# Kernel optimization log

Hardware: AMD Instinct MI355X
Metric: run time of the kernel (lower is better)

The kernel has to match this reference:

```python
import jax, jax.numpy as jnp
import numpy as np

K = 24            # kNN neighbors per DynamicEdgeConv (includes self, dist 0)
N_PER_GRAPH = 128 # uniform nodes per graph
N_GRAPHS = 128
N_IN = 16
HID = 128
N_OUT = 6


def _knn_idx(xg, k):
    # xg: [G, N, D] -> indices of k nearest neighbors per node, [G, N, k]
    sq = jnp.sum(xg * xg, axis=-1)                       # [G, N]
    d2 = sq[:, :, None] + sq[:, None, :] - 2.0 * jnp.einsum('gnd,gmd->gnm', xg, xg)
    _, idx = jax.lax.top_k(-d2, k)                       # smallest distances
    return idx


def _dynamic_edge_conv(xg, w, b, k=K):
    # DynamicEdgeConv: recompute kNN on current features, edge MLP on
    # [x_i, x_j - x_i], max-aggregate over neighbors.
    idx = _knn_idx(xg, k)                                # [G, N, k]
    x_j = jax.vmap(lambda v, i: v[i])(xg, idx)           # [G, N, k, D]
    x_i = xg[:, :, None, :]                              # [G, N, 1, D]
    e = jnp.concatenate([jnp.broadcast_to(x_i, x_j.shape), x_j - x_i], axis=-1)
    h = jax.nn.elu(jnp.einsum('gnkf,fh->gnkh', e, w) + b)
    return jnp.max(h, axis=2)                            # [G, N, H]


def _linear(x, w, b):
    return x @ w + b


def setup_inputs() -> dict:
    key = jax.random.key(0)
    ks = jax.random.split(key, 16)

    def W(k, fi, fo):
        return (jax.random.normal(k, (fi, fo), dtype=jnp.float32) / np.sqrt(fi)).astype(jnp.float32)

    inp = {
        'x_pf': jax.random.normal(ks[0], (N_GRAPHS * N_PER_GRAPH, N_IN), dtype=jnp.float32),
        'enc_w1': W(ks[1], N_IN, HID),  'enc_b1': jnp.zeros((HID,), jnp.float32),
        'enc_w2': W(ks[2], HID, HID),   'enc_b2': jnp.zeros((HID,), jnp.float32),
        'conv1_w': W(ks[3], 2 * HID, HID), 'conv1_b': jnp.zeros((HID,), jnp.float32),
        'conv2_w': W(ks[4], 2 * HID, HID), 'conv2_b': jnp.zeros((HID,), jnp.float32),
        'conv3_w': W(ks[5], 2 * HID, HID), 'conv3_b': jnp.zeros((HID,), jnp.float32),
        'out_w1': W(ks[6], HID, 64), 'out_b1': jnp.zeros((64,), jnp.float32),
        'out_w2': W(ks[7], 64, 32),  'out_b2': jnp.zeros((32,), jnp.float32),
        'out_w3': W(ks[8], 32, 32),  'out_b3': jnp.zeros((32,), jnp.float32),
        'out_w4': W(ks[9], 32, N_OUT), 'out_b4': jnp.zeros((N_OUT,), jnp.float32),
        'batch_pf': jnp.repeat(jnp.arange(N_GRAPHS, dtype=jnp.int64 if jax.config.jax_enable_x64 else jnp.int32), N_PER_GRAPH),
    }
    return inp


def reference(x_pf, enc_w1, enc_b1, enc_w2, enc_b2,
              conv1_w, conv1_b, conv2_w, conv2_b, conv3_w, conv3_b,
              out_w1, out_b1, out_w2, out_b2, out_w3, out_b3, out_w4, out_b4,
              batch_pf):
    G = x_pf.shape[0] // N_PER_GRAPH
    # pf_encode: Linear -> ELU -> Linear -> ELU
    h = jax.nn.elu(_linear(x_pf, enc_w1, enc_b1))
    h = jax.nn.elu(_linear(h, enc_w2, enc_b2))
    hg = h.reshape(G, N_PER_GRAPH, HID)  # uniform graphs; batch_pf = repeat(arange(G))
    hg = _dynamic_edge_conv(hg, conv1_w, conv1_b)
    hg = _dynamic_edge_conv(hg, conv2_w, conv2_b)
    hg = _dynamic_edge_conv(hg, conv3_w, conv3_b)
    # global_add_pool over nodes of each graph
    pooled = jnp.sum(hg, axis=1)                          # [G, HID]
    o = jax.nn.elu(_linear(pooled, out_w1, out_b1))
    o = jax.nn.elu(_linear(o, out_w2, out_b2))
    o = jax.nn.elu(_linear(o, out_w3, out_b3))
    o = _linear(o, out_w4, out_b4)
    return (o, batch_pf)
```

## Files before the change

### kernel.cpp

```cpp
#include <hip/hip_runtime.h>
#include <hip/hip_fp16.h>
#include <hip/hip_bf16.h>
#include <cmath>

#define G_NUM 128
#define NPTS  128
#define FDIM  128
#define KNNK  24
#define NTOT  (G_NUM*NPTS)

typedef short s8v __attribute__((ext_vector_type(8)));
typedef float f32x4 __attribute__((ext_vector_type(4)));

__device__ __forceinline__ float eluf(float x){ return x > 0.0f ? x : expm1f(x); }

__device__ __forceinline__ unsigned short f2bf(float f) {
    unsigned int u = __float_as_uint(f);
    unsigned int r = (u + 0x7fffu + ((u >> 16) & 1u)) >> 16;
    return (unsigned short)r;
}
__device__ __forceinline__ float bf2f(unsigned short b) {
    return __uint_as_float(((unsigned int)b) << 16);
}

__global__ void prep_kernel(const float* __restrict__ w1, const float* __restrict__ w2,
                            const float* __restrict__ w3, const float* __restrict__ ew2,
                            const float* __restrict__ b1, const float* __restrict__ b2,
                            const float* __restrict__ b3,
                            unsigned short* __restrict__ wcatT,
                            unsigned short* __restrict__ enc2T,
                            float* __restrict__ bias,
                            const int* __restrict__ bpf,
                            float* __restrict__ out)
{
    int e = blockIdx.x * 256 + threadIdx.x;
    if (e < 16384) out[768 + e] = (float)bpf[e];
    if (e < 98304) {
        int l = e >> 15;
        int r = e & 32767;
        int k = r >> 8;
        int n = r & 255;
        const float* w = (l == 0) ? w1 : ((l == 1) ? w2 : w3);
        float v = (n < 128) ? (w[k * 128 + n] - w[(128 + k) * 128 + n])
                            : w[(128 + k) * 128 + (n - 128)];
        wcatT[l * 32768 + n * 128 + k] = f2bf(v);
    } else if (e < 114688) {
        int i = e - 98304;
        int k = i >> 7, n = i & 127;
        enc2T[n * 128 + k] = f2bf(ew2[k * 128 + n]);
    } else if (e < 115456) {
        int j = e - 114688;
        int l = j >> 8, c = j & 255;
        const float* b = (l == 0) ? b1 : ((l == 1) ? b2 : b3);
        bias[l * 256 + c] = (c < 128) ? b[c] : 0.0f;
    }
}

#define E_XS  0
#define E_W1  4352
#define E_A   12544
__global__ __launch_bounds__(512) void enc_fused(const float* __restrict__ x_pf,
                                                 const float* __restrict__ w1,
                                                 const float* __restrict__ b1,
                                                 const unsigned short* __restrict__ e2T,
                                                 const float* __restrict__ b2,
                                                 float* __restrict__ hout)
{
    __shared__ char smc[28928];
    float* xs  = (float*)(smc + E_XS);
    float* ws1 = (float*)(smc + E_W1);
    const int tid = threadIdx.x;
    const int m0 = blockIdx.x * 64;

    for (int e = tid; e < 1024; e += 512) {
        int m = e >> 4, k = e & 15;
        xs[m * 17 + k] = x_pf[(size_t)(m0 + m) * 16 + k];
    }
    for (int e = tid; e < 2048; e += 512) ws1[e] = w1[e];
    __syncthreads();

    {
        const int h = tid & 127, mg = tid >> 7;
        float bb = b1[h];
        #pragma unroll
        for (int i = 0; i < 16; ++i) {
            int m = mg * 16 + i;
            float a = bb;
            #pragma unroll
            for (int k = 0; k < 16; ++k) a += xs[m * 17 + k] * ws1[k * 128 + h];
            a = eluf(a);
            int byte = (m * 256 + h * 2) ^ ((m & 15) << 4);
            *reinterpret_cast<unsigned short*>(smc + E_A + byte) = f2bf(a);
        }
    }
    __syncthreads();

    {
        const int l = tid & 63, w = tid >> 6;
        const int lr = l & 15, lg = l >> 4;
        const int mt = w >> 1, nh = w & 1;
        f32x4 acc[4] = {};
        #pragma unroll
        for (int ks = 0; ks < 4; ++ks) {
            int row = mt * 16 + lr;
            int abyte = (row * 256 + ks * 64 + lg * 16) ^ ((row & 15) << 4);
            s8v a_f = *reinterpret_cast<const s8v*>(smc + E_A + abyte);
            #pragma unroll
            for (int ni = 0; ni < 4; ++ni) {
                int n = nh * 64 + ni * 16 + lr;
                s8v b = *reinterpret_cast<const s8v*>(e2T + n * 128 + ks * 32 + lg * 8);
                acc[ni] = __builtin_amdgcn_mfma_f32_16x16x32_bf16(a_f, b, acc[ni], 0, 0, 0);
            }
        }
        #pragma unroll
        for (int ni = 0; ni < 4; ++ni) {
            int n = nh * 64 + ni * 16 + lr;
            float bl = b2[n];
            #pragma unroll
            for (int q = 0; q < 4; ++q)
                hout[(size_t)(m0 + mt * 16 + lg * 4 + q) * 128 + n] = eluf(acc[ni][q] + bl);
        }
    }
}

__global__ __launch_bounds__(256) void cgemm(const float* __restrict__ A,
                                             const unsigned short* __restrict__ Bt,
                                             const float* __restrict__ bias,
                                             float* __restrict__ a_out,
                                             unsigned int* __restrict__ c16)
{
    extern __shared__ char smc[];
    const int tid = threadIdx.x;
    const int m0 = blockIdx.x * 128;
    const unsigned short* Btg = Bt + (size_t)blockIdx.y * 16384;

    for (int e = tid; e < 4096; e += 256) {
        int m = e >> 5, q = e & 31;
        float4 v = *reinterpret_cast<const float4*>(&A[(size_t)(m0 + m) * 128 + 4 * q]);
        ushort4 p;
        p.x = f2bf(v.x); p.y = f2bf(v.y); p.z = f2bf(v.z); p.w = f2bf(v.w);
        int byte = (m * 256 + q * 8) ^ ((m & 15) << 4);
        *reinterpret_cast<ushort4*>(smc + byte) = p;
    }
    for (int e = tid; e < 2048; e += 256) {
        int n = e >> 4, q = e & 15;
        uint4 v = *reinterpret_cast<const uint4*>(Btg + n * 128 + q * 8);
        int byte = (n * 256 + q * 16) ^ ((n & 15) << 4);
        *reinterpret_cast<uint4*>(smc + 32768 + byte) = v;
    }
    __syncthreads();

    const int l = tid & 63, w = tid >> 6;
    const int wr = w >> 1, wc = w & 1;
    const int lr = l & 15, lg = l >> 4;

    f32x4 acc[4][4] = {};
    #pragma unroll
    for (int ks = 0; ks < 4; ++ks) {
        s8v a_f[4], b_f[4];
        #pragma unroll
        for (int mi = 0; mi < 4; ++mi) {
            int row = wr * 64 + mi * 16 + lr;
            int byte = (row * 256 + ks * 64 + lg * 16) ^ ((row & 15) << 4);
            a_f[mi] = *reinterpret_cast<const s8v*>(smc + byte);
        }
        #pragma unroll
        for (int ni = 0; ni < 4; ++ni) {
            int n = wc * 64 + ni * 16 + lr;
            int byte = (n * 256 + ks * 64 + lg * 16) ^ ((n & 15) << 4);
            b_f[ni] = *reinterpret_cast<const s8v*>(smc + 32768 + byte);
        }
        #pragma unroll
        for (int mi = 0; mi < 4; ++mi)
            #pragma unroll
            for (int ni = 0; ni < 4; ++ni)
                acc[mi][ni] = __builtin_amdgcn_mfma_f32_16x16x32_bf16(
                    a_f[mi], b_f[ni], acc[mi][ni], 0, 0, 0);
    }

    if (blockIdx.y == 0) {
        float bl[4];
        #pragma unroll
        for (int ni = 0; ni < 4; ++ni) bl[ni] = bias[wc * 64 + ni * 16 + lr];
        #pragma unroll
        for (int mi = 0; mi < 4; ++mi) {
            int rbase = m0 + wr * 64 + mi * 16 + lg * 4;
            #pragma unroll
            for (int ni = 0; ni < 4; ++ni) {
                int col = wc * 64 + ni * 16 + lr;
                #pragma unroll
                for (int q = 0; q < 4; ++q)
                    a_out[(size_t)(rbase + q) * 128 + col] = acc[mi][ni][q] + bl[ni];
            }
        }
    } else {
        #pragma unroll
        for (int mi = 0; mi < 4; ++mi) {
            int rbase = m0 + wr * 64 + mi * 16 + lg * 4;
            #pragma unroll
            for (int ni = 0; ni < 4; ++ni) {
                int col = wc * 64 + ni * 16 + lr;
                #pragma unroll
                for (int q = 0; q < 4; ++q) {
                    float v = acc[mi][ni][q];
                    float p = __shfl_xor(v, 1);
                    if (!(lr & 1)) {
                        unsigned int u =
                            ((unsigned int)__half_as_ushort(__float2half(p)) << 16)
                          |  (unsigned int)__half_as_ushort(__float2half(v));
                        c16[(size_t)(rbase + q) * 64 + (col >> 1)] = u;
                    }
                }
            }
        }
    }
}

#define CV_XHI 0
#define CV_XLO 32768
#define CV_D   32768
#define CV_PP  (32768 + 16384)
#define CV_IDX (32768 + 24576)
#define CV_SQ  65536
#define CONV_LDS 66048

template<int POOL>
__global__ __launch_bounds__(512, 4) void conv_fused(const float* __restrict__ hin,
                                                     const float* __restrict__ a_buf,
                                                     const unsigned int* __restrict__ c16,
                                                     float* __restrict__ hout,
                                                     float* __restrict__ ppool)
{
    extern __shared__ char smc[];
    float* Sq = (float*)(smc + CV_SQ);
    unsigned char* idxL = (unsigned char*)(smc + CV_IDX);
    float* pp = (float*)(smc + CV_PP);

    const int bid = blockIdx.x;
    const int g   = (bid & 7) * 16 + (bid >> 5);
    const int sub = (bid >> 3) & 3;
    const int r0  = sub * 32;
    const int tid = threadIdx.x;
    const float* hg = hin + (size_t)g * NPTS * FDIM;
    float* og = hout + (size_t)g * NPTS * FDIM;

    {
        const int m = tid >> 2;
        const int k0 = (tid & 3) * 32;
        float sq = 0.f;
        #pragma unroll
        for (int i = 0; i < 8; ++i) {
            float4 v = *reinterpret_cast<const float4*>(&hg[m * 128 + k0 + 4 * i]);
            ushort4 hi, lo;
            hi.x = f2bf(v.x); lo.x = f2bf(v.x - bf2f(hi.x));
            hi.y = f2bf(v.y); lo.y = f2bf(v.y - bf2f(hi.y));
            hi.z = f2bf(v.z); lo.z = f2bf(v.z - bf2f(hi.z));
            hi.w = f2bf(v.w); lo.w = f2bf(v.w - bf2f(hi.w));
            sq += v.x * v.x + v.y * v.y + v.z * v.z + v.w * v.w;
            int byte = (m * 256 + (k0 + 4 * i) * 2) ^ ((m & 15) << 4);
            *reinterpret_cast<ushort4*>(smc + CV_XHI + byte) = hi;
            *reinterpret_cast<ushort4*>(smc + CV_XLO + byte) = lo;
        }
        sq += __shfl_xor(sq, 1);
        sq += __shfl_xor(sq, 2);
        if ((tid & 3) == 0) Sq[m] = sq;
    }
    __syncthreads();

    const int l = tid & 63, w = tid >> 6;
    const int lr = l & 15, lg = l >> 4;

    f32x4 acc[2] = {};
    const int rt = w & 1, ct0 = w >> 1;
    const int arow = r0 + rt * 16 + lr;
    const int aswz = (arow & 15) << 4;
    #pragma unroll
    for (int ks = 0; ks < 4; ++ks) {
        int abyte = (arow * 256 + ks * 64 + lg * 16) ^ aswz;
        s8v ahi = *reinterpret_cast<const s8v*>(smc + CV_XHI + abyte);
        s8v alo = *reinterpret_cast<const s8v*>(smc + CV_XLO + abyte);
        #pragma unroll
        for (int t = 0; t < 2; ++t) {
            int brow = (ct0 + 4 * t) * 16 + lr;
            int bbyte = (brow * 256 + ks * 64 + lg * 16) ^ ((brow & 15) << 4);
            s8v bhi = *reinterpret_cast<const s8v*>(smc + CV_XHI + bbyte);
            s8v blo = *reinterpret_cast<const s8v*>(smc + CV_XLO + bbyte);
            acc[t] = __builtin_amdgcn_mfma_f32_16x16x32_bf16(alo, bhi, acc[t], 0, 0, 0);
            acc[t] = __builtin_amdgcn_mfma_f32_16x16x32_bf16(ahi, blo, acc[t], 0, 0, 0);
            acc[t] = __builtin_amdgcn_mfma_f32_16x16x32_bf16(ahi, bhi, acc[t], 0, 0, 0);
        }
    }
    float sqa[4], sqc[2];
    #pragma unroll
    for (int q = 0; q < 4; ++q) sqa[q] = Sq[r0 + rt * 16 + lg * 4 + q];
    #pragma unroll
    for (int t = 0; t < 2; ++t) sqc[t] = Sq[(ct0 + 4 * t) * 16 + lr];
    __syncthreads();

    #pragma unroll
    for (int t = 0; t < 2; ++t) {
        int col = (ct0 + 4 * t) * 16 + lr;
        #pragma unroll
        for (int q = 0; q < 4; ++q) {
            int row = rt * 16 + lg * 4 + q;
            *reinterpret_cast<float*>(smc + CV_D + ((row * 512 + col * 4) ^ ((row & 7) << 4)))
                = sqa[q] + sqc[t] - 2.f * acc[t][q];
        }
    }
    __syncthreads();

    for (int r = w * 4; r < w * 4 + 4; ++r) {
        float2 cur = *reinterpret_cast<const float2*>(
            smc + CV_D + ((r * 512 + 8 * l) ^ ((r & 7) << 4)));
        unsigned int ub0 = __float_as_uint(cur.x);
        unsigned int ub1 = __float_as_uint(cur.y);
        unsigned int u0 = (ub0 & 0x80000000u) ? ~ub0 : (ub0 | 0x80000000u);
        unsigned int u1 = (ub1 & 0x80000000u) ? ~ub1 : (ub1 | 0x80000000u);

        bool c0 = true, c1 = true, in0 = false, in1 = false;
        int need = KNNK;
        for (int b = 31; b >= 0; --b) {
            bool z0 = c0 && !((u0 >> b) & 1u);
            bool z1 = c1 && !((u1 >> b) & 1u);
            int cnt = __popcll(__ballot(z0)) + __popcll(__ballot(z1));
            if (cnt > need) { c0 = z0; c1 = z1; }
            else if (cnt == need) { in0 |= z0; in1 |= z1; need = 0; break; }
            else { in0 |= z0; in1 |= z1; need -= cnt;
                   c0 = c0 && !z0; c1 = c1 && !z1; }
        }
        if (need > 0) {
            unsigned long long m0 = __ballot(c0), m1 = __ballot(c1);
            unsigned long long below = (1ull << l) - 1ull;
            int rk0 = __popcll(m0 & below) + __popcll(m1 & below);
            int rk1 = rk0 + (int)((m0 >> l) & 1ull);
            in0 = in0 || (c0 && rk0 < need);
            in1 = in1 || (c1 && rk1 < need);
        }
        unsigned long long f0 = __ballot(in0), f1 = __ballot(in1);
        int cnt0 = __popcll(f0);
        unsigned long long below = (1ull << l) - 1ull;
        if (in0) idxL[r * KNNK + __popcll(f0 & below)] = (unsigned char)(2 * l);
        if (in1) idxL[r * KNNK + cnt0 + __popcll(f1 & below)] = (unsigned char)(2 * l + 1);
    }

    {
        const int hh = l >> 5, jl = l & 31;
        const float* ag = a_buf + ((size_t)g * 128 + r0) * 128;
        const unsigned int* cg = c16 + (size_t)g * 128 * 64;
        float4 ps = {0.f, 0.f, 0.f, 0.f};
        #pragma unroll
        for (int u = 0; u < 2; ++u) {
            const int r = w * 4 + 2 * u + hh;
            const unsigned char* il = &idxL[r * KNNK];
            float4 av = *reinterpret_cast<const float4*>(&ag[r * 128 + 4 * jl]);
            float mc0 = -3.0e38f, mc1 = -3.0e38f, mc2 = -3.0e38f, mc3 = -3.0e38f;
            #pragma unroll
            for (int t = 0; t < KNNK; t += 4) {
                int p0 = il[t], p1 = il[t + 1], p2 = il[t + 2], p3 = il[t + 3];
                uint2 a = *reinterpret_cast<const uint2*>(&cg[(size_t)p0 * 64 + 2 * jl]);
                uint2 b = *reinterpret_cast<const uint2*>(&cg[(size_t)p1 * 64 + 2 * jl]);
                uint2 c = *reinterpret_cast<const uint2*>(&cg[(size_t)p2 * 64 + 2 * jl]);
                uint2 d = *reinterpret_cast<const uint2*>(&cg[(size_t)p3 * 64 + 2 * jl]);
                mc0 = fmaxf(fmaxf(mc0,
                        __half2float(__ushort_as_half((unsigned short)(a.x & 0xffffu)))),
                        fmaxf(__half2float(__ushort_as_half((unsigned short)(b.x & 0xffffu))),
                              fmaxf(__half2float(__ushort_as_half((unsigned short)(c.x & 0xffffu))),
                                    __half2float(__ushort_as_half((unsigned short)(d.x & 0xffffu))))));
                mc1 = fmaxf(fmaxf(mc1,
                        __half2float(__ushort_as_half((unsigned short)(a.x >> 16)))),
                        fmaxf(__half2float(__ushort_as_half((unsigned short)(b.x >> 16))),
                              fmaxf(__half2float(__ushort_as_half((unsigned short)(c.x >> 16))),
                                    __half2float(__ushort_as_half((unsigned short)(d.x >> 16))))));
                mc2 = fmaxf(fmaxf(mc2,
                        __half2float(__ushort_as_half((unsigned short)(a.y & 0xffffu)))),
                        fmaxf(__half2float(__ushort_as_half((unsigned short)(b.y & 0xffffu))),
                              fmaxf(__half2float(__ushort_as_half((unsigned short)(c.y & 0xffffu))),
                                    __half2float(__ushort_as_half((unsigned short)(d.y & 0xffffu))))));
                mc3 = fmaxf(fmaxf(mc3,
                        __half2float(__ushort_as_half((unsigned short)(a.y >> 16)))),
                        fmaxf(__half2float(__ushort_as_half((unsigned short)(b.y >> 16))),
                              fmaxf(__half2float(__ushort_as_half((unsigned short)(c.y >> 16))),
                                    __half2float(__ushort_as_half((unsigned short)(d.y >> 16))))));
            }
            float4 o;
            o.x = eluf(av.x + mc0);
            o.y = eluf(av.y + mc1);
            o.z = eluf(av.z + mc2);
            o.w = eluf(av.w + mc3);
            if (!POOL) {
                *reinterpret_cast<float4*>(&og[(r0 + r) * 128 + 4 * jl]) = o;
            } else {
                ps.x += o.x; ps.y += o.y; ps.z += o.z; ps.w += o.w;
            }
        }
        if (POOL) {
            *reinterpret_cast<float4*>(&pp[(w * 2 + hh) * 128 + 4 * jl]) = ps;
            __syncthreads();
            if (tid < 128) {
                float s = 0.f;
                #pragma unroll 8
                for (int rg = 0; rg < 16; ++rg) s += pp[rg * 128 + tid];
                ppool[(size_t)(g * 4 + sub) * 128 + tid] = s;
            }
        }
    }
}

__global__ __launch_bounds__(128) void head_kernel(const float* __restrict__ ppool,
        const float* __restrict__ w1, const float* __restrict__ b1,
        const float* __restrict__ w2, const float* __restrict__ b2,
        const float* __restrict__ w3, const float* __restrict__ b3,
        const float* __restrict__ w4, const float* __restrict__ b4,
        float* __restrict__ out)
{
    __shared__ float pooled[128], s1[64], s2[32], s3[32];
    const int g = blockIdx.x, t = threadIdx.x;
    pooled[t] = ppool[(size_t)(4 * g) * 128 + t] + ppool[(size_t)(4 * g + 1) * 128 + t]
              + ppool[(size_t)(4 * g + 2) * 128 + t] + ppool[(size_t)(4 * g + 3) * 128 + t];
    __syncthreads();
    if (t < 64) {
        float a = b1[t];
        #pragma unroll 8
        for (int k = 0; k < 128; ++k) a += pooled[k] * w1[k * 64 + t];
        s1[t] = eluf(a);
    }
    __syncthreads();
    if (t < 32) {
        float a = b2[t];
        #pragma unroll 8
        for (int k = 0; k < 64; ++k) a += s1[k] * w2[k * 32 + t];
        s2[t] = eluf(a);
    }
    __syncthreads();
    if (t < 32) {
        float a = b3[t];
        #pragma unroll 8
        for (int k = 0; k < 32; ++k) a += s2[k] * w3[k * 32 + t];
        s3[t] = eluf(a);
    }
    __syncthreads();
    if (t < 6) {
        float a = b4[t];
        #pragma unroll 8
        for (int k = 0; k < 32; ++k) a += s3[k] * w4[k * 6 + t];
        out[g * 6 + t] = a;
    }
}

extern "C" void kernel_launch(void* const* d_in, const int* in_sizes, int n_in,
                              void* d_out, int out_size, void* d_ws, size_t ws_size,
                              hipStream_t stream)
{
    const float* x_pf   = (const float*)d_in[0];
    const float* enc_w1 = (const float*)d_in[1];
    const float* enc_b1 = (const float*)d_in[2];
    const float* enc_w2 = (const float*)d_in[3];
    const float* enc_b2 = (const float*)d_in[4];
    const float* c1w = (const float*)d_in[5];
    const float* c1b = (const float*)d_in[6];
    const float* c2w = (const float*)d_in[7];
    const float* c2b = (const float*)d_in[8];
    const float* c3w = (const float*)d_in[9];
    const float* c3b = (const float*)d_in[10];
    const float* o_w1 = (const float*)d_in[11];
    const float* o_b1 = (const float*)d_in[12];
    const float* o_w2 = (const float*)d_in[13];
    const float* o_b2 = (const float*)d_in[14];
    const float* o_w3 = (const float*)d_in[15];
    const float* o_b3 = (const float*)d_in[16];
    const float* o_w4 = (const float*)d_in[17];
    const float* o_b4 = (const float*)d_in[18];
    const int*   bpf  = (const int*)d_in[19];
    float* out = (float*)d_out;

    float* ws    = (float*)d_ws;
    float* h_a   = ws;
    float* h_b   = h_a + (size_t)NTOT * FDIM;
    float* a_buf = h_b + (size_t)NTOT * FDIM;
    unsigned int* c16 = (unsigned int*)(a_buf + (size_t)NTOT * FDIM);
    float* ppool = (float*)(c16 + (size_t)NTOT * 64);
    unsigned short* wcatT = (unsigned short*)(ppool + 512 * 128);
    unsigned short* enc2T = wcatT + 3 * 32768;
    float* biasF = (float*)(enc2T + 16384);

    prep_kernel<<<451, 256, 0, stream>>>(c1w, c2w, c3w, enc_w2,
                                         c1b, c2b, c3b, wcatT, enc2T, biasF,
                                         bpf, out);

    enc_fused<<<NTOT / 64, 512, 0, stream>>>(x_pf, enc_w1, enc_b1,
                                             enc2T, enc_b2, h_a);

    float* hc = h_a;
    float* hn = h_b;
    for (int lyr = 0; lyr < 3; ++lyr) {
        cgemm<<<dim3(NTOT / 128, 2), 256, 65536, stream>>>(
            hc, wcatT + (size_t)lyr * 32768, biasF + lyr * 256, a_buf, c16);
        if (lyr < 2)
            conv_fused<0><<<512, 512, CONV_LDS, stream>>>(hc, a_buf, c16, hn, ppool);
        else
            conv_fused<1><<<512, 512, CONV_LDS, stream>>>(hc, a_buf, c16, hn, ppool);
        float* t = hc; hc = hn; hn = t;
    }

    head_kernel<<<G_NUM, 128, 0, stream>>>(ppool, o_w1, o_b1, o_w2, o_b2,
                                           o_w3, o_b3, o_w4, o_b4, out);
}
```

Before: 265.7 us.

## Fuse per-layer edge GEMM into conv kernel with fp16 self-term buffer

Removes the separate cgemm launch for each layer. Inside conv_all, warps 0-3 compute the kNN distance tile while warps 4-7 compute the neighbour projection C for the whole graph and the self projection A for the block's rows. The A term is now stored as packed fp16 instead of fp32, which cuts the buffer traffic in the gather stage. In exchange, each of the four sub-blocks of a graph recomputes and rewrites the full-graph C projection. That adds redundant MFMA work and benign duplicate global writes, and the block relies on __syncthreads for visibility of its own global writes before the gather.

Result: no change. 261.3 us (-1.7%).

```diff
diff --git a/kernel.cpp b/kernel.cpp
--- a/kernel.cpp
+++ b/kernel.cpp
@@ -1,6 +1,5 @@
 #include <hip/hip_runtime.h>
 #include <hip/hip_fp16.h>
-#include <hip/hip_bf16.h>
 #include <cmath>
 
 #define G_NUM 128
@@ -22,6 +21,8 @@
 __device__ __forceinline__ float bf2f(unsigned short b) {
     return __uint_as_float(((unsigned int)b) << 16);
 }
+__device__ __forceinline__ unsigned short f2h(float f){ return __half_as_ushort(__float2half(f)); }
+__device__ __forceinline__ float h2f(unsigned short h){ return __half2float(__ushort_as_half(h)); }
 
 __global__ void prep_kernel(const float* __restrict__ w1, const float* __restrict__ w2,
                             const float* __restrict__ w3, const float* __restrict__ ew2,
@@ -123,113 +124,22 @@
     }
 }
 
-__global__ __launch_bounds__(256) void cgemm(const float* __restrict__ A,
-                                             const unsigned short* __restrict__ Bt,
-                                             const float* __restrict__ bias,
-                                             float* __restrict__ a_out,
-                                             unsigned int* __restrict__ c16)
-{
-    extern __shared__ char smc[];
-    const int tid = threadIdx.x;
-    const int m0 = blockIdx.x * 128;
-    const unsigned short* Btg = Bt + (size_t)blockIdx.y * 16384;
-
-    for (int e = tid; e < 4096; e += 256) {
-        int m = e >> 5, q = e & 31;
-        float4 v = *reinterpret_cast<const float4*>(&A[(size_t)(m0 + m) * 128 + 4 * q]);
-        ushort4 p;
-        p.x = f2bf(v.x); p.y = f2bf(v.y); p.z = f2bf(v.z); p.w = f2bf(v.w);
-        int byte = (m * 256 + q * 8) ^ ((m & 15) << 4);
-        *reinterpret_cast<ushort4*>(smc + byte) = p;
-    }
-    for (int e = tid; e < 2048; e += 256) {
-        int n = e >> 4, q = e & 15;
-        uint4 v = *reinterpret_cast<const uint4*>(Btg + n * 128 + q * 8);
-        int byte = (n * 256 + q * 16) ^ ((n & 15) << 4);
-        *reinterpret_cast<uint4*>(smc + 32768 + byte) = v;
-    }
-    __syncthreads();
-
-    const int l = tid & 63, w = tid >> 6;
-    const int wr = w >> 1, wc = w & 1;
-    const int lr = l & 15, lg = l >> 4;
-
-    f32x4 acc[4][4] = {};
-    #pragma unroll
-    for (int ks = 0; ks < 4; ++ks) {
-        s8v a_f[4], b_f[4];
-        #pragma unroll
-        for (int mi = 0; mi < 4; ++mi) {
-            int row = wr * 64 + mi * 16 + lr;
-            int byte = (row * 256 + ks * 64 + lg * 16) ^ ((row & 15) << 4);
-            a_f[mi] = *reinterpret_cast<const s8v*>(smc + byte);
-        }
-        #pragma unroll
-        for (int ni = 0; ni < 4; ++ni) {
-            int n = wc * 64 + ni * 16 + lr;
-            int byte = (n * 256 + ks * 64 + lg * 16) ^ ((n & 15) << 4);
-            b_f[ni] = *reinterpret_cast<const s8v*>(smc + 32768 + byte);
-        }
-        #pragma unroll
-        for (int mi = 0; mi < 4; ++mi)
-            #pragma unroll
-            for (int ni = 0; ni < 4; ++ni)
-                acc[mi][ni] = __builtin_amdgcn_mfma_f32_16x16x32_bf16(
-                    a_f[mi], b_f[ni], acc[mi][ni], 0, 0, 0);
-    }
-
-    if (blockIdx.y == 0) {
-        float bl[4];
-        #pragma unroll
-        for (int ni = 0; ni < 4; ++ni) bl[ni] = bias[wc * 64 + ni * 16 + lr];
-        #pragma unroll
-        for (int mi = 0; mi < 4; ++mi) {
-            int rbase = m0 + wr * 64 + mi * 16 + lg * 4;
-            #pragma unroll
-            for (int ni = 0; ni < 4; ++ni) {
-                int col = wc * 64 + ni * 16 + lr;
-                #pragma unroll
-                for (int q = 0; q < 4; ++q)
-                    a_out[(size_t)(rbase + q) * 128 + col] = acc[mi][ni][q] + bl[ni];
-            }
-        }
-    } else {
-        #pragma unroll
-        for (int mi = 0; mi < 4; ++mi) {
-            int rbase = m0 + wr * 64 + mi * 16 + lg * 4;
-            #pragma unroll
-            for (int ni = 0; ni < 4; ++ni) {
-                int col = wc * 64 + ni * 16 + lr;
-                #pragma unroll
-                for (int q = 0; q < 4; ++q) {
-                    float v = acc[mi][ni][q];
-                    float p = __shfl_xor(v, 1);
-                    if (!(lr & 1)) {
-                        unsigned int u =
-                            ((unsigned int)__half_as_ushort(__float2half(p)) << 16)
-                          |  (unsigned int)__half_as_ushort(__float2half(v));
-                        c16[(size_t)(rbase + q) * 64 + (col >> 1)] = u;
-                    }
-                }
-            }
-        }
-    }
-}
-
 #define CV_XHI 0
 #define CV_XLO 32768
 #define CV_D   32768
-#define CV_PP  (32768 + 16384)
-#define CV_IDX (32768 + 24576)
-#define CV_SQ  65536
-#define CONV_LDS 66048
+#define CV_PP  49152
+#define CV_IDX 65536
+#define CV_SQ  66304
+#define CONV_LDS 66816
 
 template<int POOL>
-__global__ __launch_bounds__(512, 4) void conv_fused(const float* __restrict__ hin,
-                                                     const float* __restrict__ a_buf,
-                                                     const unsigned int* __restrict__ c16,
-                                                     float* __restrict__ hout,
-                                                     float* __restrict__ ppool)
+__global__ __launch_bounds__(512, 4) void conv_all(const float* __restrict__ hin,
+                                                   const unsigned short* __restrict__ wT,
+                                                   const float* __restrict__ bias,
+                                                   float* __restrict__ hout,
+                                                   unsigned int* __restrict__ a16,
+                                                   unsigned int* __restrict__ c16,
+                                                   float* __restrict__ ppool)
 {
     extern __shared__ char smc[];
     float* Sq = (float*)(smc + CV_SQ);
@@ -237,12 +147,13 @@
     float* pp = (float*)(smc + CV_PP);
 
     const int bid = blockIdx.x;
-    const int g   = (bid & 7) * 16 + (bid >> 5);
+    const int g   = (bid & 7) | ((bid >> 5) << 3);
     const int sub = (bid >> 3) & 3;
     const int r0  = sub * 32;
     const int tid = threadIdx.x;
     const float* hg = hin + (size_t)g * NPTS * FDIM;
-    float* og = hout + (size_t)g * NPTS * FDIM;
+    unsigned int* a16g = a16 + (size_t)g * NPTS * 64;
+    unsigned int* c16g = c16 + (size_t)g * NPTS * 64;
 
     {
         const int m = tid >> 2;
@@ -270,41 +181,124 @@
     const int l = tid & 63, w = tid >> 6;
     const int lr = l & 15, lg = l >> 4;
 
-    f32x4 acc[2] = {};
-    const int rt = w & 1, ct0 = w >> 1;
-    const int arow = r0 + rt * 16 + lr;
-    const int aswz = (arow & 15) << 4;
-    #pragma unroll
-    for (int ks = 0; ks < 4; ++ks) {
-        int abyte = (arow * 256 + ks * 64 + lg * 16) ^ aswz;
-        s8v ahi = *reinterpret_cast<const s8v*>(smc + CV_XHI + abyte);
-        s8v alo = *reinterpret_cast<const s8v*>(smc + CV_XLO + abyte);
-        #pragma unroll
-        for (int t = 0; t < 2; ++t) {
-            int brow = (ct0 + 4 * t) * 16 + lr;
-            int bbyte = (brow * 256 + ks * 64 + lg * 16) ^ ((brow & 15) << 4);
-            s8v bhi = *reinterpret_cast<const s8v*>(smc + CV_XHI + bbyte);
-            s8v blo = *reinterpret_cast<const s8v*>(smc + CV_XLO + bbyte);
-            acc[t] = __builtin_amdgcn_mfma_f32_16x16x32_bf16(alo, bhi, acc[t], 0, 0, 0);
-            acc[t] = __builtin_amdgcn_mfma_f32_16x16x32_bf16(ahi, blo, acc[t], 0, 0, 0);
-            acc[t] = __builtin_amdgcn_mfma_f32_16x16x32_bf16(ahi, bhi, acc[t], 0, 0, 0);
-        }
-    }
-    float sqa[4], sqc[2];
-    #pragma unroll
-    for (int q = 0; q < 4; ++q) sqa[q] = Sq[r0 + rt * 16 + lg * 4 + q];
-    #pragma unroll
-    for (int t = 0; t < 2; ++t) sqc[t] = Sq[(ct0 + 4 * t) * 16 + lr];
-    __syncthreads();
-
-    #pragma unroll
-    for (int t = 0; t < 2; ++t) {
-        int col = (ct0 + 4 * t) * 16 + lr;
-        #pragma unroll
-        for (int q = 0; q < 4; ++q) {
-            int row = rt * 16 + lg * 4 + q;
-            *reinterpret_cast<float*>(smc + CV_D + ((row * 512 + col * 4) ^ ((row & 7) << 4)))
-                = sqa[q] + sqc[t] - 2.f * acc[t][q];
+    f32x4 dacc[4] = {};
+    float sqa[4], sqc[4];
+    if (w < 4) {
+        const int rt = w >> 1;
+        const int ch = w & 1;
+        const int arow = r0 + rt * 16 + lr;
+        const int aswz = (arow & 15) << 4;
+        #pragma unroll
+        for (int ks = 0; ks < 4; ++ks) {
+            int abyte = (arow * 256 + ks * 64 + lg * 16) ^ aswz;
+            s8v ahi = *reinterpret_cast<const s8v*>(smc + CV_XHI + abyte);
+            s8v alo = *reinterpret_cast<const s8v*>(smc + CV_XLO + abyte);
+            #pragma unroll
+            for (int t = 0; t < 4; ++t) {
+                int brow = (ch * 4 + t) * 16 + lr;
+                int bbyte = (brow * 256 + ks * 64 + lg * 16) ^ ((brow & 15) << 4);
+                s8v bhi = *reinterpret_cast<const s8v*>(smc + CV_XHI + bbyte);
+                s8v blo = *reinterpret_cast<const s8v*>(smc + CV_XLO + bbyte);
+                dacc[t] = __builtin_amdgcn_mfma_f32_16x16x32_bf16(alo, bhi, dacc[t], 0, 0, 0);
+                dacc[t] = __builtin_amdgcn_mfma_f32_16x16x32_bf16(ahi, blo, dacc[t], 0, 0, 0);
+                dacc[t] = __builtin_amdgcn_mfma_f32_16x16x32_bf16(ahi, bhi, dacc[t], 0, 0, 0);
+            }
+        }
+        #pragma unroll
+        for (int q = 0; q < 4; ++q) sqa[q] = Sq[r0 + rt * 16 + lg * 4 + q];
+        #pragma unroll
+        for (int t = 0; t < 4; ++t) sqc[t] = Sq[(ch * 4 + t) * 16 + lr];
+    } else {
+        const int w4 = w - 4;
+        {
+            f32x4 cacc[2][8] = {};
+            #pragma unroll
+            for (int ks = 0; ks < 4; ++ks) {
+                s8v a_f[2];
+                #pragma unroll
+                for (int m2 = 0; m2 < 2; ++m2) {
+                    int row = (2 * w4 + m2) * 16 + lr;
+                    int byte = (row * 256 + ks * 64 + lg * 16) ^ ((row & 15) << 4);
+                    a_f[m2] = *reinterpret_cast<const s8v*>(smc + CV_XHI + byte);
+                }
+                #pragma unroll
+                for (int ni = 0; ni < 8; ++ni) {
+                    int n = 128 + ni * 16 + lr;
+                    s8v b = *reinterpret_cast<const s8v*>(wT + n * 128 + ks * 32 + lg * 8);
+                    #pragma unroll
+                    for (int m2 = 0; m2 < 2; ++m2)
+                        cacc[m2][ni] = __builtin_amdgcn_mfma_f32_16x16x32_bf16(
+                            a_f[m2], b, cacc[m2][ni], 0, 0, 0);
+                }
+            }
+            #pragma unroll
+            for (int m2 = 0; m2 < 2; ++m2)
+                #pragma unroll
+                for (int ni = 0; ni < 8; ++ni)
+                    #pragma unroll
+                    for (int q = 0; q < 4; ++q) {
+                        float v = cacc[m2][ni][q];
+                        float p = __shfl_xor(v, 1);
+                        if (!(lr & 1)) {
+                            unsigned int u = ((unsigned int)f2h(p) << 16) | f2h(v);
+                            int j = (2 * w4 + m2) * 16 + lg * 4 + q;
+                            c16g[(size_t)j * 64 + ((ni * 16 + lr) >> 1)] = u;
+                        }
+                    }
+        }
+        {
+            f32x4 aacc[2][2] = {};
+            #pragma unroll
+            for (int ks = 0; ks < 4; ++ks) {
+                s8v a_f[2];
+                #pragma unroll
+                for (int m2 = 0; m2 < 2; ++m2) {
+                    int row = r0 + m2 * 16 + lr;
+                    int byte = (row * 256 + ks * 64 + lg * 16) ^ ((row & 15) << 4);
+                    a_f[m2] = *reinterpret_cast<const s8v*>(smc + CV_XHI + byte);
+                }
+                #pragma unroll
+                for (int ci = 0; ci < 2; ++ci) {
+                    int n = (2 * w4 + ci) * 16 + lr;
+                    s8v b = *reinterpret_cast<const s8v*>(wT + n * 128 + ks * 32 + lg * 8);
+                    #pragma unroll
+                    for (int m2 = 0; m2 < 2; ++m2)
+                        aacc[m2][ci] = __builtin_amdgcn_mfma_f32_16x16x32_bf16(
+                            a_f[m2], b, aacc[m2][ci], 0, 0, 0);
+                }
+            }
+            #pragma unroll
+            for (int m2 = 0; m2 < 2; ++m2)
+                #pragma unroll
+                for (int ci = 0; ci < 2; ++ci) {
+                    int col = (2 * w4 + ci) * 16 + lr;
+                    float bl = bias[col];
+                    #pragma unroll
+                    for (int q = 0; q < 4; ++q) {
+                        float v = aacc[m2][ci][q] + bl;
+                        float p = __shfl_xor(v, 1);
+                        if (!(lr & 1)) {
+                            unsigned int u = ((unsigned int)f2h(p) << 16) | f2h(v);
+                            int row = r0 + m2 * 16 + lg * 4 + q;
+                            a16g[(size_t)row * 64 + (col >> 1)] = u;
+                        }
+                    }
+                }
+        }
+    }
+    __syncthreads();
+
+    if (w < 4) {
+        const int rt = w >> 1, ch = w & 1;
+        #pragma unroll
+        for (int t = 0; t < 4; ++t) {
+            int col = (ch * 4 + t) * 16 + lr;
+            #pragma unroll
+            for (int q = 0; q < 4; ++q) {
+                int row = rt * 16 + lg * 4 + q;
+                *reinterpret_cast<float*>(smc + CV_D + ((row * 512 + col * 4) ^ ((row & 7) << 4)))
+                    = sqa[q] + sqc[t] - 2.f * dacc[t][q];
+            }
         }
     }
     __syncthreads();
@@ -345,52 +339,47 @@
 
     {
         const int hh = l >> 5, jl = l & 31;
-        const float* ag = a_buf + ((size_t)g * 128 + r0) * 128;
-        const unsigned int* cg = c16 + (size_t)g * 128 * 64;
+        float* og = hout + (size_t)g * NPTS * FDIM;
         float4 ps = {0.f, 0.f, 0.f, 0.f};
         #pragma unroll
         for (int u = 0; u < 2; ++u) {
             const int r = w * 4 + 2 * u + hh;
             const unsigned char* il = &idxL[r * KNNK];
-            float4 av = *reinterpret_cast<const float4*>(&ag[r * 128 + 4 * jl]);
+            uint2 avu = *reinterpret_cast<const uint2*>(&a16g[(size_t)(r0 + r) * 64 + 2 * jl]);
             float mc0 = -3.0e38f, mc1 = -3.0e38f, mc2 = -3.0e38f, mc3 = -3.0e38f;
             #pragma unroll
             for (int t = 0; t < KNNK; t += 4) {
                 int p0 = il[t], p1 = il[t + 1], p2 = il[t + 2], p3 = il[t + 3];
-                uint2 a = *reinterpret_cast<const uint2*>(&cg[(size_t)p0 * 64 + 2 * jl]);
-                uint2 b = *reinterpret_cast<const uint2*>(&cg[(size_t)p1 * 64 + 2 * jl]);
-                uint2 c = *reinterpret_cast<const uint2*>(&cg[(size_t)p2 * 64 + 2 * jl]);
-                uint2 d = *reinterpret_cast<const uint2*>(&cg[(size_t)p3 * 64 + 2 * jl]);
-                mc0 = fmaxf(fmaxf(mc0,
-                        __half2float(__ushort_as_half((unsigned short)(a.x & 0xffffu)))),
-                        fmaxf(__half2float(__ushort_as_half((unsigned short)(b.x & 0xffffu))),
-                              fmaxf(__half2float(__ushort_as_half((unsigned short)(c.x & 0xffffu))),
-                                    __half2float(__ushort_as_half((unsigned short)(d.x & 0xffffu))))));
-                mc1 = fmaxf(fmaxf(mc1,
-                        __half2float(__ushort_as_half((unsigned short)(a.x >> 16)))),
-                        fmaxf(__half2float(__ushort_as_half((unsigned short)(b.x >> 16))),
-                              fmaxf(__half2float(__ushort_as_half((unsigned short)(c.x >> 16))),
-                                    __half2float(__ushort_as_half((unsigned short)(d.x >> 16))))));
-                mc2 = fmaxf(fmaxf(mc2,
-                        __half2float(__ushort_as_half((unsigned short)(a.y & 0xffffu)))),
-                        fmaxf(__half2float(__ushort_as_half((unsigned short)(b.y & 0xffffu))),
-                              fmaxf(__half2float(__ushort_as_half((unsigned short)(c.y & 0xffffu))),
-                                    __half2float(__ushort_as_half((unsigned short)(d.y & 0xffffu))))));
-                mc3 = fmaxf(fmaxf(mc3,
-                        __half2float(__ushort_as_half((unsigned short)(a.y >> 16)))),
-                        fmaxf(__half2float(__ushort_as_half((unsigned short)(b.y >> 16))),
-                              fmaxf(__half2float(__ushort_as_half((unsigned short)(c.y >> 16))),
-                                    __half2float(__ushort_as_half((unsigned short)(d.y >> 16))))));
-            }
-            float4 o;
-            o.x = eluf(av.x + mc0);
-            o.y = eluf(av.y + mc1);
-            o.z = eluf(av.z + mc2);
-            o.w = eluf(av.w + mc3);
+                uint2 a = *reinterpret_cast<const uint2*>(&c16g[(size_t)p0 * 64 + 2 * jl]);
+                uint2 b = *reinterpret_cast<const uint2*>(&c16g[(size_t)p1 * 64 + 2 * jl]);
+                uint2 c = *reinterpret_cast<const uint2*>(&c16g[(size_t)p2 * 64 + 2 * jl]);
+                uint2 d = *reinterpret_cast<const uint2*>(&c16g[(size_t)p3 * 64 + 2 * jl]);
+                mc0 = fmaxf(fmaxf(mc0, h2f((unsigned short)(a.x & 0xffffu))),
+                        fmaxf(h2f((unsigned short)(b.x & 0xffffu)),
+                              fmaxf(h2f((unsigned short)(c.x & 0xffffu)),
+                                    h2f((unsigned short)(d.x & 0xffffu)))));
+                mc1 = fmaxf(fmaxf(mc1, h2f((unsigned short)(a.x >> 16))),
+                        fmaxf(h2f((unsigned short)(b.x >> 16)),
+                              fmaxf(h2f((unsigned short)(c.x >> 16)),
+                                    h2f((unsigned short)(d.x >> 16)))));
+                mc2 = fmaxf(fmaxf(mc2, h2f((unsigned short)(a.y & 0xffffu))),
+                        fmaxf(h2f((unsigned short)(b.y & 0xffffu)),
+                              fmaxf(h2f((unsigned short)(c.y & 0xffffu)),
+                                    h2f((unsigned short)(d.y & 0xffffu)))));
+                mc3 = fmaxf(fmaxf(mc3, h2f((unsigned short)(a.y >> 16))),
+                        fmaxf(h2f((unsigned short)(b.y >> 16)),
+                              fmaxf(h2f((unsigned short)(c.y >> 16)),
+                                    h2f((unsigned short)(d.y >> 16)))));
+            }
+            float o0 = eluf(h2f((unsigned short)(avu.x & 0xffffu)) + mc0);
+            float o1 = eluf(h2f((unsigned short)(avu.x >> 16)) + mc1);
+            float o2 = eluf(h2f((unsigned short)(avu.y & 0xffffu)) + mc2);
+            float o3 = eluf(h2f((unsigned short)(avu.y >> 16)) + mc3);
             if (!POOL) {
-                *reinterpret_cast<float4*>(&og[(r0 + r) * 128 + 4 * jl]) = o;
+                float4 o = {o0, o1, o2, o3};
+                *reinterpret_cast<float4*>(&og[(size_t)(r0 + r) * 128 + 4 * jl]) = o;
             } else {
-                ps.x += o.x; ps.y += o.y; ps.z += o.z; ps.w += o.w;
+                ps.x += o0; ps.y += o1; ps.z += o2; ps.w += o3;
             }
         }
         if (POOL) {
@@ -473,11 +462,10 @@
     const int*   bpf  = (const int*)d_in[19];
     float* out = (float*)d_out;
 
-    float* ws    = (float*)d_ws;
-    float* h_a   = ws;
-    float* h_b   = h_a + (size_t)NTOT * FDIM;
-    float* a_buf = h_b + (size_t)NTOT * FDIM;
-    unsigned int* c16 = (unsigned int*)(a_buf + (size_t)NTOT * FDIM);
+    float* h_a = (float*)d_ws;
+    float* h_b = h_a + (size_t)NTOT * FDIM;
+    unsigned int* a16 = (unsigned int*)(h_b + (size_t)NTOT * FDIM);
+    unsigned int* c16 = a16 + (size_t)NTOT * 64;
     float* ppool = (float*)(c16 + (size_t)NTOT * 64);
     unsigned short* wcatT = (unsigned short*)(ppool + 512 * 128);
     unsigned short* enc2T = wcatT + 3 * 32768;
@@ -493,12 +481,12 @@
     float* hc = h_a;
     float* hn = h_b;
     for (int lyr = 0; lyr < 3; ++lyr) {
-        cgemm<<<dim3(NTOT / 128, 2), 256, 65536, stream>>>(
-            hc, wcatT + (size_t)lyr * 32768, biasF + lyr * 256, a_buf, c16);
         if (lyr < 2)
-            conv_fused<0><<<512, 512, CONV_LDS, stream>>>(hc, a_buf, c16, hn, ppool);
+            conv_all<0><<<512, 512, CONV_LDS, stream>>>(
+                hc, wcatT + (size_t)lyr * 32768, biasF + lyr * 256, hn, a16, c16, ppool);
         else
-            conv_fused<1><<<512, 512, CONV_LDS, stream>>>(hc, a_buf, c16, hn, ppool);
+            conv_all<1><<<512, 512, CONV_LDS, stream>>>(
+                hc, wcatT + (size_t)lyr * 32768, biasF + lyr * 256, hn, a16, c16, ppool);
         float* t = hc; hc = hn; hn = t;
     }
 
```
